# Performance work log

Measured on AMD Instinct MI355X. Metric: run time of the kernel, lower is better.

Reference implementation:

```python
import jax, jax.numpy as jnp
import numpy as np

B = 8          # number of simulations in the batch
K = 3          # torch_geometric knn_interpolate default k
EPS = 1e-16    # clamp floor for squared distances (matches torch_geometric)


def setup_inputs() -> dict:
    key = jax.random.key(0)
    k1, k2, k3 = jax.random.split(key, 3)
    N_mesh, C, D = 65536, 64, 2
    G_total = 16384
    x = jax.random.normal(k1, (N_mesh, C), dtype=jnp.float32)
    mesh_pos = jax.random.uniform(k2, (N_mesh, D), dtype=jnp.float32)
    grid_pos = jax.random.uniform(k3, (G_total, D), dtype=jnp.float32)
    # uniform number of mesh points per batch element (sorted, contiguous)
    batch_idx = jnp.repeat(jnp.arange(B, dtype=jnp.int64), N_mesh // B)
    return {"x": x, "mesh_pos": mesh_pos, "grid_pos": grid_pos, "batch_idx": batch_idx}


def reference(x, mesh_pos, grid_pos, batch_idx):
    # x: [N_mesh, C] mesh features; mesh_pos: [N_mesh, D]; grid_pos: [B*G, D]
    # batch_idx: [N_mesh] sorted, uniform counts per batch (see setup_inputs)
    N, C = x.shape
    M = N // B                      # mesh points per batch
    G = grid_pos.shape[0] // B      # grid points per batch
    xb = x.reshape(B, M, C)
    mp = mesh_pos.reshape(B, M, -1)
    gp = grid_pos.reshape(B, G, -1)

    # squared pairwise distances per batch: [B, G, M]
    g2 = jnp.sum(gp * gp, axis=-1)                      # [B, G]
    m2 = jnp.sum(mp * mp, axis=-1)                      # [B, M]
    d2 = g2[:, :, None] + m2[:, None, :] - 2.0 * jnp.einsum('bgd,bmd->bgm', gp, mp)

    # k nearest mesh points for each grid point
    neg_d2, idx = jax.lax.top_k(-d2, K)                 # idx: [B, G, K]
    w = 1.0 / jnp.clip(-neg_d2, EPS)                    # inverse squared-distance weights

    # gather neighbor features: [B, G, K, C]
    xk = xb[jnp.arange(B)[:, None, None], idx]

    out = jnp.einsum('bgk,bgkc->bgc', w, xk) / jnp.sum(w, axis=-1, keepdims=True)
    return out.reshape(B * G, C)
```

## Files before the change

### kernel.cpp

```cpp
#include <hip/hip_runtime.h>


#define BLK 256
#define LPG 32
#define PPB 8
#define NTB 1024
#define NB 32
#define NBINS (NB * NB)
#define PADIDX 0x7FFFFFFF
#define MARGIN 1e-4f

__global__ void bin_all(const float* __restrict__ mesh_pos,
                        int* __restrict__ starts,
                        float4* __restrict__ sxyi,
                        int M)
{
#pragma clang fp contract(off)
    __shared__ int h[NBINS];
    __shared__ int wsum[16];
    __shared__ int woff[17];
    extern __shared__ char dsm[];
    float2* stage = (float2*)dsm;
    int*    sidl  = (int*)(dsm + (size_t)M * sizeof(float2));

    const int b = blockIdx.x, t = threadIdx.x;

    h[t] = 0;
    __syncthreads();

    const float2* mp = (const float2*)mesh_pos + (size_t)b * M;
    for (int n = t; n < M; n += NTB) {
        const float2 p = mp[n];
        const int bx = max(0, min((int)(p.x * (float)NB), NB - 1));
        const int by = max(0, min((int)(p.y * (float)NB), NB - 1));
        atomicAdd(&h[by * NB + bx], 1);
    }
    __syncthreads();

    const int v = h[t];
    int sc = v;
    #pragma unroll
    for (int off = 1; off < 64; off <<= 1) {
        int nv = __shfl_up(sc, off, 64);
        if ((t & 63) >= off) sc += nv;
    }
    if ((t & 63) == 63) wsum[t >> 6] = sc;
    __syncthreads();
    if (t == 0) {
        int acc = 0;
        #pragma unroll
        for (int i = 0; i < 16; ++i) { woff[i] = acc; acc += wsum[i]; }
        woff[16] = acc;
    }
    __syncthreads();
    const int excl = woff[t >> 6] + sc - v;
    starts[b * (NBINS + 1) + t] = excl;
    if (t == 0) starts[b * (NBINS + 1) + NBINS] = woff[16];
    __syncthreads();
    h[t] = excl;
    __syncthreads();

    for (int n = t; n < M; n += NTB) {
        const float2 p = mp[n];
        const int bx = max(0, min((int)(p.x * (float)NB), NB - 1));
        const int by = max(0, min((int)(p.y * (float)NB), NB - 1));
        const int pos = atomicAdd(&h[by * NB + bx], 1);
        stage[pos] = p;
        sidl[pos]  = n;
    }
    __syncthreads();

    for (int n = t; n < M; n += NTB) {
        const float2 p = stage[n];
        const float m2 = (p.x * p.x) + (p.y * p.y);
        sxyi[(size_t)b * M + n] =
            make_float4(p.x, p.y, m2, __int_as_float(sidl[n]));
    }
}

#define LEX_INSERT(d2, idx)                                                  \
    if ((d2) < t2 || ((d2) == t2 && (idx) < i2)) {                           \
        if ((d2) < t1 || ((d2) == t1 && (idx) < i1)) {                       \
            t2 = t1; i2 = i1;                                                \
            if ((d2) < t0 || ((d2) == t0 && (idx) < i0)) {                   \
                t1 = t0; i1 = i0; t0 = (d2); i0 = (idx);                     \
            } else { t1 = (d2); i1 = (idx); }                                \
        } else { t2 = (d2); i2 = (idx); }                                    \
    }

#define MERGE3_LEVEL(off)                                                    \
    {                                                                        \
        const float o0 = __shfl_xor(t0, (off), 64);                          \
        const int   p0_ = __shfl_xor(i0, (off), 64);                         \
        const float o1 = __shfl_xor(t1, (off), 64);                          \
        const int   p1_ = __shfl_xor(i1, (off), 64);                         \
        const float o2 = __shfl_xor(t2, (off), 64);                          \
        const int   p2_ = __shfl_xor(i2, (off), 64);                         \
        float c0d, d0d; int c0i, d0i;                                        \
        if (o0 < t0 || (o0 == t0 && p0_ < i0))                               \
             { c0d = o0; c0i = p0_; d0d = t0; d0i = i0; }                    \
        else { c0d = t0; c0i = i0; d0d = o0; d0i = p0_; }                    \
        float c1d; int c1i;                                                  \
        if (o1 < t1 || (o1 == t1 && p1_ < i1)) { c1d = o1; c1i = p1_; }      \
        else                                   { c1d = t1; c1i = i1; }      \
        float c2d; int c2i;                                                  \
        if (o2 < t2 || (o2 == t2 && p2_ < i2)) { c2d = o2; c2i = p2_; }      \
        else                                   { c2d = t2; c2i = i2; }      \
        float r1d, l1d; int r1i, l1i;                                        \
        if (c1d < d0d || (c1d == d0d && c1i < d0i))                          \
             { r1d = c1d; r1i = c1i; l1d = d0d; l1i = d0i; }                 \
        else { r1d = d0d; r1i = d0i; l1d = c1d; l1i = c1i; }                 \
        float r2d; int r2i;                                                  \
        if (c2d < l1d || (c2d == l1d && c2i < l1i)) { r2d = c2d; r2i = c2i; }\
        else                                        { r2d = l1d; r2i = l1i; }\
        t0 = c0d; i0 = c0i; t1 = r1d; i1 = r1i; t2 = r2d; i2 = r2i;          \
    }

__global__ void knn_search(const float* __restrict__ x,
                           const float* __restrict__ grid_pos,
                           const float4* __restrict__ sxyi,
                           const int* __restrict__ starts,
                           float* __restrict__ out,
                           int M, int G)
{
#pragma clang fp contract(off)
    const int tid  = threadIdx.x;
    const int lb   = (blockIdx.x >> 3) + (blockIdx.x & 7) * 256;
    const int g0   = lb * PPB;
    const int b    = g0 / G;
    const int pt   = tid >> 5;
    const int li   = tid & (LPG - 1);
    const int lane = tid & 63;

    const int g = g0 + pt;
    const float2 gp = ((const float2*)grid_pos)[g];
    const float gx = gp.x, gy = gp.y;
    const float g2 = (gx * gx) + (gy * gy);

    const int gbx = max(0, min((int)(gx * (float)NB), NB - 1));
    const int gby = max(0, min((int)(gy * (float)NB), NB - 1));
    const int bxlo = max(gbx - 1, 0), bxhi = min(gbx + 1, NB - 1);
    const int bylo = max(gby - 1, 0), byhi = min(gby + 1, NB - 1);

    const int* st = starts + b * (NBINS + 1);
    const float4* bxyi = sxyi + (size_t)b * M;

    const int lo0 = st[bylo * NB + bxlo];
    const int hi0 = st[bylo * NB + bxhi + 1];
    int lo1 = 0, hi1 = 0, lo2 = 0, hi2 = 0;
    if (bylo + 1 <= byhi) { lo1 = st[(bylo + 1) * NB + bxlo];
                            hi1 = st[(bylo + 1) * NB + bxhi + 1]; }
    if (bylo + 2 <= byhi) { lo2 = st[(bylo + 2) * NB + bxlo];
                            hi2 = st[(bylo + 2) * NB + bxhi + 1]; }

    const int c0  = hi0 - lo0;
    const int c01 = c0 + (hi1 - lo1);
    const int T   = c01 + (hi2 - lo2);

    float t0 = 1e30f, t1 = 1e30f, t2 = 1e30f;
    int   i0 = PADIDX, i1 = PADIDX, i2 = PADIDX;

    for (int L = li; L < T; L += LPG) {
        int sp;
        if (L < c0)       sp = lo0 + L;
        else if (L < c01) sp = lo1 + (L - c0);
        else              sp = lo2 + (L - c01);
        const float4 v = bxyi[sp];
        const float p0  = gx * v.x;
        const float dot = fmaf(gy, v.y, p0);
        const float t   = g2 + v.z;
        const float d2  = fmaf(-2.0f, dot, t);
        const int   idx = __float_as_int(v.w);
        LEX_INSERT(d2, idx)
    }

    MERGE3_LEVEL(1)  MERGE3_LEVEL(2)  MERGE3_LEVEL(4)
    MERGE3_LEVEL(8)  MERGE3_LEVEL(16)
    float wd0 = t0, wd1 = t1, wd2 = t2;
    int   wi0 = i0, wi1 = i1, wi2 = i2;

    const float w = 1.0f / (float)NB;
    const float dl = (bxlo > 0)      ? (gx - (float)bxlo * w)       : 1e30f;
    const float dr = (bxhi < NB - 1) ? ((float)(bxhi + 1) * w - gx) : 1e30f;
    const float dn = (bylo > 0)      ? (gy - (float)bylo * w)       : 1e30f;
    const float dt = (byhi < NB - 1) ? ((float)(byhi + 1) * w - gy) : 1e30f;
    const float bdd = fminf(fminf(dl, dr), fminf(dn, dt));
    const float bd2 = bdd * bdd;
    const bool need = (li == 0) && !(wd2 + MARGIN < bd2);

    unsigned long long mask = __ballot(need);
    while (mask) {
        const int l = __builtin_ctzll(mask); mask &= mask - 1;
        const int ptf = ((tid & ~63) + l) >> 5;
        const float2 fgp = ((const float2*)grid_pos)[g0 + ptf];
        const float fgx = fgp.x, fgy = fgp.y;
        const float fg2 = (fgx * fgx) + (fgy * fgy);
        t0 = 1e30f; t1 = 1e30f; t2 = 1e30f;
        i0 = PADIDX; i1 = PADIDX; i2 = PADIDX;
        for (int j = lane; j < M; j += 64) {
            const float4 v = bxyi[j];
            const float p0  = fgx * v.x;
            const float dot = fmaf(fgy, v.y, p0);
            const float t   = fg2 + v.z;
            const float d2  = fmaf(-2.0f, dot, t);
            const int   idx = __float_as_int(v.w);
            LEX_INSERT(d2, idx)
        }
        MERGE3_LEVEL(1)  MERGE3_LEVEL(2)  MERGE3_LEVEL(4)
        MERGE3_LEVEL(8)  MERGE3_LEVEL(16) MERGE3_LEVEL(32)
        if (pt == ptf) { wd0 = t0; wi0 = i0; wd1 = t1; wi1 = i1;
                         wd2 = t2; wi2 = i2; }
    }

    const int wv = tid >> 6;
    const size_t rowBase = (size_t)b * M * 64;
    #pragma unroll
    for (int q = 0; q < 2; ++q) {
        const int src = q << 5;
        const float a0 = __shfl(wd0, src, 64);
        const float a1 = __shfl(wd1, src, 64);
        const float a2 = __shfl(wd2, src, 64);
        const int   J0 = __shfl(wi0, src, 64);
        const int   J1 = __shfl(wi1, src, 64);
        const int   J2 = __shfl(wi2, src, 64);
        const float W0 = 1.0f / fmaxf(a0, 1e-16f);
        const float W1 = 1.0f / fmaxf(a1, 1e-16f);
        const float W2 = 1.0f / fmaxf(a2, 1e-16f);
        const float x0 = x[rowBase + (size_t)J0 * 64 + lane];
        const float x1 = x[rowBase + (size_t)J1 * 64 + lane];
        const float x2 = x[rowBase + (size_t)J2 * 64 + lane];
        const float num = ((W0 * x0) + (W1 * x1)) + (W2 * x2);
        const float den = (W0 + W1) + W2;
        out[(size_t)(g0 + (wv << 1) + q) * 64 + lane] = num / den;
    }
}

extern "C" void kernel_launch(void* const* d_in, const int* in_sizes, int n_in,
                              void* d_out, int out_size, void* d_ws, size_t ws_size,
                              hipStream_t stream) {
    const float* x        = (const float*)d_in[0];
    const float* mesh_pos = (const float*)d_in[1];
    const float* grid_pos = (const float*)d_in[2];

    const int N  = in_sizes[1] / 2;
    const int Gt = in_sizes[2] / 2;
    const int B  = 8;
    const int M  = N / B;
    const int G  = Gt / B;

    char* p = (char*)d_ws;
    int*    starts = (int*)p;     p += (size_t)B * (NBINS + 1) * sizeof(int);
    float4* sxyi   = (float4*)p;

    const size_t dsmBytes = (size_t)M * 12;
    bin_all   <<<B, NTB, dsmBytes, stream>>>(mesh_pos, starts, sxyi, M);
    knn_search<<<Gt / PPB, BLK, 0, stream>>>(x, grid_pos, sxyi, starts,
                                             (float*)d_out, M, G);
}
```

Before: 19.59 us.

## Split binning into parallel histogram, scan, and scatter kernels across sub-blocks

The single-block-per-batch counting sort becomes three kernels. Per-sub-block histograms run over 64 blocks, a scan kernel builds global bin starts and per-sub-block bases, and a 64-block scatter writes the sorted float4 records. This spreads work that used only 8 CUs onto many more, at the cost of two extra launches and global round-trips for the histograms. The code hard-codes M = NSUB*NTB = 8192, and the order within a bin is now nondeterministic across sub-blocks, which can change tie-breaking.

```diff
diff --git a/kernel.cpp b/kernel.cpp
--- a/kernel.cpp
+++ b/kernel.cpp
@@ -5,40 +5,44 @@
 #define LPG 32
 #define PPB 8
 #define NTB 1024
+#define NSUB 8
 #define NB 32
 #define NBINS (NB * NB)
 #define PADIDX 0x7FFFFFFF
 #define MARGIN 1e-4f
 
-__global__ void bin_all(const float* __restrict__ mesh_pos,
-                        int* __restrict__ starts,
-                        float4* __restrict__ sxyi,
-                        int M)
-{
-#pragma clang fp contract(off)
+__global__ void bin_hist(const float* __restrict__ mesh_pos,
+                         int* __restrict__ hist2, int M)
+{
     __shared__ int h[NBINS];
+    const int blk = blockIdx.x;
+    const int b = blk >> 3, s = blk & 7;
+    const int t = threadIdx.x;
+    h[t] = 0;
+    __syncthreads();
+    const float2 p = ((const float2*)mesh_pos)[(size_t)b * M + s * NTB + t];
+    const int bx = max(0, min((int)(p.x * (float)NB), NB - 1));
+    const int by = max(0, min((int)(p.y * (float)NB), NB - 1));
+    atomicAdd(&h[by * NB + bx], 1);
+    __syncthreads();
+    hist2[(blk << 10) + t] = h[t];
+}
+
+__global__ void bin_scan(const int* __restrict__ hist2,
+                         int* __restrict__ starts,
+                         int* __restrict__ base2)
+{
     __shared__ int wsum[16];
     __shared__ int woff[17];
-    extern __shared__ char dsm[];
-    float2* stage = (float2*)dsm;
-    int*    sidl  = (int*)(dsm + (size_t)M * sizeof(float2));
-
     const int b = blockIdx.x, t = threadIdx.x;
-
-    h[t] = 0;
-    __syncthreads();
-
-    const float2* mp = (const float2*)mesh_pos + (size_t)b * M;
-    for (int n = t; n < M; n += NTB) {
-        const float2 p = mp[n];
-        const int bx = max(0, min((int)(p.x * (float)NB), NB - 1));
-        const int by = max(0, min((int)(p.y * (float)NB), NB - 1));
-        atomicAdd(&h[by * NB + bx], 1);
-    }
-    __syncthreads();
-
-    const int v = h[t];
-    int sc = v;
+    int hv[NSUB];
+    int tot = 0;
+    #pragma unroll
+    for (int s = 0; s < NSUB; ++s) {
+        hv[s] = hist2[((b * NSUB + s) << 10) + t];
+        tot += hv[s];
+    }
+    int sc = tot;
     #pragma unroll
     for (int off = 1; off < 64; off <<= 1) {
         int nv = __shfl_up(sc, off, 64);
@@ -53,29 +57,36 @@
         woff[16] = acc;
     }
     __syncthreads();
-    const int excl = woff[t >> 6] + sc - v;
+    const int excl = woff[t >> 6] + sc - tot;
     starts[b * (NBINS + 1) + t] = excl;
     if (t == 0) starts[b * (NBINS + 1) + NBINS] = woff[16];
-    __syncthreads();
-    h[t] = excl;
-    __syncthreads();
-
-    for (int n = t; n < M; n += NTB) {
-        const float2 p = mp[n];
-        const int bx = max(0, min((int)(p.x * (float)NB), NB - 1));
-        const int by = max(0, min((int)(p.y * (float)NB), NB - 1));
-        const int pos = atomicAdd(&h[by * NB + bx], 1);
-        stage[pos] = p;
-        sidl[pos]  = n;
-    }
-    __syncthreads();
-
-    for (int n = t; n < M; n += NTB) {
-        const float2 p = stage[n];
-        const float m2 = (p.x * p.x) + (p.y * p.y);
-        sxyi[(size_t)b * M + n] =
-            make_float4(p.x, p.y, m2, __int_as_float(sidl[n]));
-    }
+    int run = excl;
+    #pragma unroll
+    for (int s = 0; s < NSUB; ++s) {
+        base2[((b * NSUB + s) << 10) + t] = run;
+        run += hv[s];
+    }
+}
+
+__global__ void bin_scatter(const float* __restrict__ mesh_pos,
+                            const int* __restrict__ base2,
+                            float4* __restrict__ sxyi,
+                            int M)
+{
+#pragma clang fp contract(off)
+    __shared__ int cur[NBINS];
+    const int blk = blockIdx.x;
+    const int b = blk >> 3, s = blk & 7;
+    const int t = threadIdx.x;
+    cur[t] = base2[(blk << 10) + t];
+    __syncthreads();
+    const int n = s * NTB + t;
+    const float2 p = ((const float2*)mesh_pos)[(size_t)b * M + n];
+    const int bx = max(0, min((int)(p.x * (float)NB), NB - 1));
+    const int by = max(0, min((int)(p.y * (float)NB), NB - 1));
+    const float m2 = (p.x * p.x) + (p.y * p.y);
+    const int pos = atomicAdd(&cur[by * NB + bx], 1);
+    sxyi[(size_t)b * M + pos] = make_float4(p.x, p.y, m2, __int_as_float(n));
 }
 
 #define LEX_INSERT(d2, idx)                                                  \
@@ -249,11 +260,14 @@
     const int G  = Gt / B;
 
     char* p = (char*)d_ws;
+    int*    hist2  = (int*)p;     p += (size_t)B * NSUB * NBINS * sizeof(int);
+    int*    base2  = (int*)p;     p += (size_t)B * NSUB * NBINS * sizeof(int);
     int*    starts = (int*)p;     p += (size_t)B * (NBINS + 1) * sizeof(int);
     float4* sxyi   = (float4*)p;
 
-    const size_t dsmBytes = (size_t)M * 12;
-    bin_all   <<<B, NTB, dsmBytes, stream>>>(mesh_pos, starts, sxyi, M);
-    knn_search<<<Gt / PPB, BLK, 0, stream>>>(x, grid_pos, sxyi, starts,
-                                             (float*)d_out, M, G);
-}
+    bin_hist   <<<B * NSUB, NTB, 0, stream>>>(mesh_pos, hist2, M);
+    bin_scan   <<<B, NTB, 0, stream>>>(hist2, starts, base2);
+    bin_scatter<<<B * NSUB, NTB, 0, stream>>>(mesh_pos, base2, sxyi, M);
+    knn_search <<<Gt / PPB, BLK, 0, stream>>>(x, grid_pos, sxyi, starts,
+                                              (float*)d_out, M, G);
+}
```

Result: slower. 23.71 us (+21.0%).

## Replace per-batch counting-sort binning with fixed-capacity bins via global atomics

Applied to the files above, without the earlier changes.

Swaps the single-block-per-batch counting sort (histogram, scan, scatter) for a fully parallel fill into fixed-capacity bins of 32 slots, using global atomics after a memset. The search kernel now visits the 3x3 neighbour bins with one lane per slot instead of a flattened loop over the prefix ranges. A bin that overflows sends that point to the brute-force fallback, which now reads the raw mesh positions. This targets the serial 8-block binning kernel, at the cost of an extra memset, global atomic contention, and nondeterministic ordering within each bin.

```diff
diff --git a/kernel.cpp b/kernel.cpp
--- a/kernel.cpp
+++ b/kernel.cpp
@@ -4,78 +4,29 @@
 #define BLK 256
 #define LPG 32
 #define PPB 8
-#define NTB 1024
 #define NB 32
 #define NBINS (NB * NB)
+#define CAP 32
 #define PADIDX 0x7FFFFFFF
 #define MARGIN 1e-4f
 
-__global__ void bin_all(const float* __restrict__ mesh_pos,
-                        int* __restrict__ starts,
-                        float4* __restrict__ sxyi,
-                        int M)
+__global__ void bin_fill(const float* __restrict__ mesh_pos,
+                         int* __restrict__ counts,
+                         float4* __restrict__ binArr,
+                         int M)
 {
 #pragma clang fp contract(off)
-    __shared__ int h[NBINS];
-    __shared__ int wsum[16];
-    __shared__ int woff[17];
-    extern __shared__ char dsm[];
-    float2* stage = (float2*)dsm;
-    int*    sidl  = (int*)(dsm + (size_t)M * sizeof(float2));
-
-    const int b = blockIdx.x, t = threadIdx.x;
-
-    h[t] = 0;
-    __syncthreads();
-
-    const float2* mp = (const float2*)mesh_pos + (size_t)b * M;
-    for (int n = t; n < M; n += NTB) {
-        const float2 p = mp[n];
-        const int bx = max(0, min((int)(p.x * (float)NB), NB - 1));
-        const int by = max(0, min((int)(p.y * (float)NB), NB - 1));
-        atomicAdd(&h[by * NB + bx], 1);
-    }
-    __syncthreads();
-
-    const int v = h[t];
-    int sc = v;
-    #pragma unroll
-    for (int off = 1; off < 64; off <<= 1) {
-        int nv = __shfl_up(sc, off, 64);
-        if ((t & 63) >= off) sc += nv;
-    }
-    if ((t & 63) == 63) wsum[t >> 6] = sc;
-    __syncthreads();
-    if (t == 0) {
-        int acc = 0;
-        #pragma unroll
-        for (int i = 0; i < 16; ++i) { woff[i] = acc; acc += wsum[i]; }
-        woff[16] = acc;
-    }
-    __syncthreads();
-    const int excl = woff[t >> 6] + sc - v;
-    starts[b * (NBINS + 1) + t] = excl;
-    if (t == 0) starts[b * (NBINS + 1) + NBINS] = woff[16];
-    __syncthreads();
-    h[t] = excl;
-    __syncthreads();
-
-    for (int n = t; n < M; n += NTB) {
-        const float2 p = mp[n];
-        const int bx = max(0, min((int)(p.x * (float)NB), NB - 1));
-        const int by = max(0, min((int)(p.y * (float)NB), NB - 1));
-        const int pos = atomicAdd(&h[by * NB + bx], 1);
-        stage[pos] = p;
-        sidl[pos]  = n;
-    }
-    __syncthreads();
-
-    for (int n = t; n < M; n += NTB) {
-        const float2 p = stage[n];
-        const float m2 = (p.x * p.x) + (p.y * p.y);
-        sxyi[(size_t)b * M + n] =
-            make_float4(p.x, p.y, m2, __int_as_float(sidl[n]));
-    }
+    const int n = blockIdx.x * BLK + threadIdx.x;
+    const int b = n / M;
+    const float2 p = ((const float2*)mesh_pos)[n];
+    const int bx = max(0, min((int)(p.x * (float)NB), NB - 1));
+    const int by = max(0, min((int)(p.y * (float)NB), NB - 1));
+    const float m2 = (p.x * p.x) + (p.y * p.y);
+    const int bin = b * NBINS + by * NB + bx;
+    const int slot = atomicAdd(&counts[bin], 1);
+    if (slot < CAP)
+        binArr[(size_t)bin * CAP + slot] =
+            make_float4(p.x, p.y, m2, __int_as_float(n - b * M));
 }
 
 #define LEX_INSERT(d2, idx)                                                  \
@@ -118,8 +69,9 @@
 
 __global__ void knn_search(const float* __restrict__ x,
                            const float* __restrict__ grid_pos,
-                           const float4* __restrict__ sxyi,
-                           const int* __restrict__ starts,
+                           const float* __restrict__ mesh_pos,
+                           const int* __restrict__ counts,
+                           const float4* __restrict__ binArr,
                            float* __restrict__ out,
                            int M, int G)
 {
@@ -142,36 +94,34 @@
     const int bxlo = max(gbx - 1, 0), bxhi = min(gbx + 1, NB - 1);
     const int bylo = max(gby - 1, 0), byhi = min(gby + 1, NB - 1);
 
-    const int* st = starts + b * (NBINS + 1);
-    const float4* bxyi = sxyi + (size_t)b * M;
-
-    const int lo0 = st[bylo * NB + bxlo];
-    const int hi0 = st[bylo * NB + bxhi + 1];
-    int lo1 = 0, hi1 = 0, lo2 = 0, hi2 = 0;
-    if (bylo + 1 <= byhi) { lo1 = st[(bylo + 1) * NB + bxlo];
-                            hi1 = st[(bylo + 1) * NB + bxhi + 1]; }
-    if (bylo + 2 <= byhi) { lo2 = st[(bylo + 2) * NB + bxlo];
-                            hi2 = st[(bylo + 2) * NB + bxhi + 1]; }
-
-    const int c0  = hi0 - lo0;
-    const int c01 = c0 + (hi1 - lo1);
-    const int T   = c01 + (hi2 - lo2);
+    const int*    cnts = counts + b * NBINS;
+    const float4* barr = binArr + (size_t)b * NBINS * CAP;
 
     float t0 = 1e30f, t1 = 1e30f, t2 = 1e30f;
     int   i0 = PADIDX, i1 = PADIDX, i2 = PADIDX;
-
-    for (int L = li; L < T; L += LPG) {
-        int sp;
-        if (L < c0)       sp = lo0 + L;
-        else if (L < c01) sp = lo1 + (L - c0);
-        else              sp = lo2 + (L - c01);
-        const float4 v = bxyi[sp];
-        const float p0  = gx * v.x;
-        const float dot = fmaf(gy, v.y, p0);
-        const float t   = g2 + v.z;
-        const float d2  = fmaf(-2.0f, dot, t);
-        const int   idx = __float_as_int(v.w);
-        LEX_INSERT(d2, idx)
+    int   over = 0;
+
+    #pragma unroll
+    for (int dy = -1; dy <= 1; ++dy) {
+        const int ry = gby + dy;
+        const bool vy = (ry >= 0) && (ry < NB);
+        #pragma unroll
+        for (int dx = -1; dx <= 1; ++dx) {
+            const int rx = gbx + dx;
+            const bool vv = vy && (rx >= 0) && (rx < NB);
+            const int bin = vv ? (ry * NB + rx) : 0;
+            const int cnt = vv ? cnts[bin] : 0;
+            over |= (cnt > CAP);
+            if (li < min(cnt, CAP)) {
+                const float4 v = barr[(size_t)bin * CAP + li];
+                const float p0  = gx * v.x;
+                const float dot = fmaf(gy, v.y, p0);
+                const float t   = g2 + v.z;
+                const float d2  = fmaf(-2.0f, dot, t);
+                const int   idx = __float_as_int(v.w);
+                LEX_INSERT(d2, idx)
+            }
+        }
     }
 
     MERGE3_LEVEL(1)  MERGE3_LEVEL(2)  MERGE3_LEVEL(4)
@@ -186,8 +136,9 @@
     const float dt = (byhi < NB - 1) ? ((float)(byhi + 1) * w - gy) : 1e30f;
     const float bdd = fminf(fminf(dl, dr), fminf(dn, dt));
     const float bd2 = bdd * bdd;
-    const bool need = (li == 0) && !(wd2 + MARGIN < bd2);
-
+    const bool need = (li == 0) && (over || !(wd2 + MARGIN < bd2));
+
+    const float2* mp2 = (const float2*)mesh_pos + (size_t)b * M;
     unsigned long long mask = __ballot(need);
     while (mask) {
         const int l = __builtin_ctzll(mask); mask &= mask - 1;
@@ -198,12 +149,13 @@
         t0 = 1e30f; t1 = 1e30f; t2 = 1e30f;
         i0 = PADIDX; i1 = PADIDX; i2 = PADIDX;
         for (int j = lane; j < M; j += 64) {
-            const float4 v = bxyi[j];
-            const float p0  = fgx * v.x;
-            const float dot = fmaf(fgy, v.y, p0);
-            const float t   = fg2 + v.z;
+            const float2 mpt = mp2[j];
+            const float m2  = (mpt.x * mpt.x) + (mpt.y * mpt.y);
+            const float p0  = fgx * mpt.x;
+            const float dot = fmaf(fgy, mpt.y, p0);
+            const float t   = fg2 + m2;
             const float d2  = fmaf(-2.0f, dot, t);
-            const int   idx = __float_as_int(v.w);
+            const int   idx = j;
             LEX_INSERT(d2, idx)
         }
         MERGE3_LEVEL(1)  MERGE3_LEVEL(2)  MERGE3_LEVEL(4)
@@ -249,11 +201,11 @@
     const int G  = Gt / B;
 
     char* p = (char*)d_ws;
-    int*    starts = (int*)p;     p += (size_t)B * (NBINS + 1) * sizeof(int);
-    float4* sxyi   = (float4*)p;
-
-    const size_t dsmBytes = (size_t)M * 12;
-    bin_all   <<<B, NTB, dsmBytes, stream>>>(mesh_pos, starts, sxyi, M);
-    knn_search<<<Gt / PPB, BLK, 0, stream>>>(x, grid_pos, sxyi, starts,
-                                             (float*)d_out, M, G);
+    int*    counts = (int*)p;     p += (size_t)B * NBINS * sizeof(int);
+    float4* binArr = (float4*)p;
+
+    hipMemsetAsync(counts, 0, (size_t)B * NBINS * sizeof(int), stream);
+    bin_fill  <<<N / BLK, BLK, 0, stream>>>(mesh_pos, counts, binArr, M);
+    knn_search<<<Gt / PPB, BLK, 0, stream>>>(x, grid_pos, mesh_pos, counts,
+                                             binArr, (float*)d_out, M, G);
 }
```

Measured after the change: 25.29 us. 29.1% more time.
